# Optimization experiments

Hardware: AMD Instinct MI355X
Metric: run time of the kernel (lower is better)

The kernel has to match this reference:

```python
import jax, jax.numpy as jnp
import numpy as np

D = 8  # sheaf block size


def setup_inputs() -> dict:
    key = jax.random.key(0)
    k1, k2, k3 = jax.random.split(key, 3)
    n, e = 1024, 32768
    x = jax.random.normal(k1, (n, D), dtype=jnp.float32)
    edge_index = jax.random.randint(k2, (2, e), 0, n, dtype=jnp.int64)
    # Phi: PyG MLP(num_layers=1, bias=False) == Linear(D, D*D, bias=False), weight [out, in]
    W = jax.random.normal(k3, (D * D, D), dtype=jnp.float32) * (1.0 / np.sqrt(D))
    return {"x": x, "edge_index": edge_index, "W": W}


def reference(x, edge_index, W):
    src, dst = edge_index[0], edge_index[1]
    # sym=True branch: |x_i - x_j| per edge  -> [e, D]
    x_in = jnp.abs(x[src] - x[dst])
    # single linear layer, no bias -> [e, D*D] -> [e, D, D]
    R_tmp = (x_in @ W.T).reshape(-1, D, D)
    n = x.shape[0]
    # dense n x n x D x D output; torch uses empty + indexed assign, we use zeros + scatter-set
    R = jnp.zeros((n, n, D, D), dtype=x.dtype).at[src, dst].set(R_tmp)
    return R
```

## Files before the change

### kernel.cpp

```cpp
#include <hip/hip_runtime.h>

#define D 8

__global__ void claim_ws_kernel(const int* __restrict__ src,
                                const int* __restrict__ dst,
                                int* __restrict__ ws, int n, int e) {
    int k = blockIdx.x * blockDim.x + threadIdx.x;
    if (k >= e) return;
    atomicMax(&ws[src[k] * n + dst[k]], k + 1);
}

__global__ void fused_out_kernel(const float* __restrict__ x,
                                 const int* __restrict__ src,
                                 const int* __restrict__ dst,
                                 const float* __restrict__ W,
                                 const int* __restrict__ ws,
                                 float4* __restrict__ out4,
                                 int n, int e, int ntiles) {
    int gid = blockIdx.x * blockDim.x + threadIdx.x;
    int tile = gid >> 4;
    int t = gid & 15;
    if (tile >= ntiles) return;

    int claim = ws[tile];
    float4 r = make_float4(0.f, 0.f, 0.f, 0.f);

    if (claim >= 1 && claim <= e) {
        int k = claim - 1;
        int s = src[k], d = dst[k];
        if (s * n + d == tile) {
            const float* xs = x + s * D;
            const float* xd = x + d * D;
            float diff[D];
#pragma unroll
            for (int i = 0; i < D; ++i) diff[i] = fabsf(xs[i] - xd[i]);
            float acc[4];
#pragma unroll
            for (int j = 0; j < 4; ++j) {
                const float* w = W + (t * 4 + j) * D;
                float a = 0.f;
#pragma unroll
                for (int i = 0; i < D; ++i) a += diff[i] * w[i];
                acc[j] = a;
            }
            r.x = acc[0]; r.y = acc[1]; r.z = acc[2]; r.w = acc[3];
        }
    }
    out4[gid] = r;
}


__global__ void zero_out_kernel(float4* __restrict__ out4, int n4) {
    int i = blockIdx.x * blockDim.x + threadIdx.x;
    if (i < n4) out4[i] = make_float4(0.f, 0.f, 0.f, 0.f);
}

__global__ void claim_out_kernel(const int* __restrict__ src,
                                 const int* __restrict__ dst,
                                 int* __restrict__ out_i, int n, int e) {
    int k = blockIdx.x * blockDim.x + threadIdx.x;
    if (k >= e) return;
    long long pair = (long long)src[k] * n + dst[k];
    atomicMax(&out_i[pair * 64], k + 1);
}

__global__ void scatter_out_kernel(const float* __restrict__ x,
                                   const int* __restrict__ src,
                                   const int* __restrict__ dst,
                                   const float* __restrict__ W,
                                   float* __restrict__ out, int n, int e) {
    int gid = blockIdx.x * blockDim.x + threadIdx.x;
    int k = gid >> 6;
    int o = gid & 63;
    if (k >= e) return;
    int s = src[k], d = dst[k];
    long long base = ((long long)s * n + d) * 64;
    int claim = __float_as_int(out[base]);
    if (claim != k + 1) return;
    const float* xs = x + s * D;
    const float* xd = x + d * D;
    const float* w = W + o * D;
    float a = 0.f;
#pragma unroll
    for (int i = 0; i < D; ++i) a += fabsf(xs[i] - xd[i]) * w[i];
    out[base + o] = a;
}

extern "C" void kernel_launch(void* const* d_in, const int* in_sizes, int n_in,
                              void* d_out, int out_size, void* d_ws, size_t ws_size,
                              hipStream_t stream) {
    const float* x  = (const float*)d_in[0];
    const int*   ei = (const int*)d_in[1];
    const float* W  = (const float*)d_in[2];

    int n = in_sizes[0] / D;
    int e = in_sizes[1] / 2;
    const int* src = ei;
    const int* dst = ei + e;

    int ntiles = out_size / 64;
    int n4 = out_size / 4;

    if (ws_size >= (size_t)ntiles * sizeof(int)) {
        int* ws = (int*)d_ws;
        {
            int threads = 256, blocks = (e + threads - 1) / threads;
            claim_ws_kernel<<<blocks, threads, 0, stream>>>(src, dst, ws, n, e);
        }
        {
            int threads = 256;
            long long total = (long long)ntiles * 16;
            int blocks = (int)((total + threads - 1) / threads);
            fused_out_kernel<<<blocks, threads, 0, stream>>>(
                x, src, dst, W, ws, (float4*)d_out, n, e, ntiles);
        }
    } else {
        {
            int threads = 256, blocks = (n4 + threads - 1) / threads;
            zero_out_kernel<<<blocks, threads, 0, stream>>>((float4*)d_out, n4);
        }
        {
            int threads = 256, blocks = (e + threads - 1) / threads;
            claim_out_kernel<<<blocks, threads, 0, stream>>>(src, dst, (int*)d_out, n, e);
        }
        {
            int threads = 256;
            long long total = (long long)e * 64;
            int blocks = (int)((total + threads - 1) / threads);
            scatter_out_kernel<<<blocks, threads, 0, stream>>>(
                x, src, dst, W, (float*)d_out, n, e);
        }
    }
}
```

Measured before the change: 289.1 us.

## Zero claim workspace explicitly and have each thread write two float4 outputs

Adds a kernel that clears the claim workspace before the atomicMax pass, so stale claims from earlier calls cannot leak into the output. The output kernel now has each thread produce two float4 words 64 apart, halving the thread count while keeping stores coalesced per wavefront. The extra zeroing pass writes a 4MB buffer, which costs time, and the two-per-thread layout is meant to raise memory-level parallelism for the 256MB output write.

```diff
diff --git a/kernel.cpp b/kernel.cpp
--- a/kernel.cpp
+++ b/kernel.cpp
@@ -1,6 +1,13 @@
 #include <hip/hip_runtime.h>
 
 #define D 8
+
+typedef int i32x4 __attribute__((ext_vector_type(4)));
+
+__global__ void zero_ws_kernel(i32x4* __restrict__ ws4, int nwords4) {
+    int i = blockIdx.x * blockDim.x + threadIdx.x;
+    if (i < nwords4) ws4[i] = (i32x4)(0, 0, 0, 0);
+}
 
 __global__ void claim_ws_kernel(const int* __restrict__ src,
                                 const int* __restrict__ dst,
@@ -10,25 +17,18 @@
     atomicMax(&ws[src[k] * n + dst[k]], k + 1);
 }
 
-__global__ void fused_out_kernel(const float* __restrict__ x,
-                                 const int* __restrict__ src,
-                                 const int* __restrict__ dst,
-                                 const float* __restrict__ W,
-                                 const int* __restrict__ ws,
-                                 float4* __restrict__ out4,
-                                 int n, int e, int ntiles) {
-    int gid = blockIdx.x * blockDim.x + threadIdx.x;
-    int tile = gid >> 4;
-    int t = gid & 15;
-    if (tile >= ntiles) return;
-
-    int claim = ws[tile];
+__device__ __forceinline__ float4 tile_word(const float* __restrict__ x,
+                                            const int* __restrict__ src,
+                                            const int* __restrict__ dst,
+                                            const float* __restrict__ W,
+                                            int claim, int idx, int n, int e) {
     float4 r = make_float4(0.f, 0.f, 0.f, 0.f);
-
     if (claim >= 1 && claim <= e) {
         int k = claim - 1;
         int s = src[k], d = dst[k];
+        int tile = idx >> 4;
         if (s * n + d == tile) {
+            int t = idx & 15;
             const float* xs = x + s * D;
             const float* xd = x + d * D;
             float diff[D];
@@ -46,7 +46,29 @@
             r.x = acc[0]; r.y = acc[1]; r.z = acc[2]; r.w = acc[3];
         }
     }
-    out4[gid] = r;
+    return r;
+}
+
+__global__ void fused_out_kernel(const float* __restrict__ x,
+                                 const int* __restrict__ src,
+                                 const int* __restrict__ dst,
+                                 const float* __restrict__ W,
+                                 const int* __restrict__ ws,
+                                 float4* __restrict__ out4,
+                                 int n, int e, int nthreads) {
+    int gid = blockIdx.x * blockDim.x + threadIdx.x;
+    if (gid >= nthreads) return;
+    int idx1 = ((gid >> 6) << 7) + (gid & 63);
+    int idx2 = idx1 + 64;
+
+    int claim1 = ws[idx1 >> 4];
+    int claim2 = ws[idx2 >> 4];
+
+    float4 r1 = tile_word(x, src, dst, W, claim1, idx1, n, e);
+    float4 r2 = tile_word(x, src, dst, W, claim2, idx2, n, e);
+
+    out4[idx1] = r1;
+    out4[idx2] = r2;
 }
 
 
@@ -104,15 +126,19 @@
     if (ws_size >= (size_t)ntiles * sizeof(int)) {
         int* ws = (int*)d_ws;
         {
+            int nwords4 = ntiles / 4;
+            int threads = 256, blocks = (nwords4 + threads - 1) / threads;
+            zero_ws_kernel<<<blocks, threads, 0, stream>>>((i32x4*)ws, nwords4);
+        }
+        {
             int threads = 256, blocks = (e + threads - 1) / threads;
             claim_ws_kernel<<<blocks, threads, 0, stream>>>(src, dst, ws, n, e);
         }
         {
-            int threads = 256;
-            long long total = (long long)ntiles * 16;
-            int blocks = (int)((total + threads - 1) / threads);
+            int nthreads = n4 / 2;
+            int threads = 256, blocks = (nthreads + threads - 1) / threads;
             fused_out_kernel<<<blocks, threads, 0, stream>>>(
-                x, src, dst, W, ws, (float4*)d_out, n, e, ntiles);
+                x, src, dst, W, ws, (float4*)d_out, n, e, nthreads);
         }
     } else {
         {
```

New measurement: 268.1 us. 7.3% less time.
